# Optimization experiments

Measured on AMD Instinct MI355X. Metric: run time of the kernel, lower is better.

## Reference

```python
import jax, jax.numpy as jnp
import numpy as np

N = 100000  # num nodes
E = 1600000  # num edges
D_IN = 64
D_OUT = 64


def setup_inputs() -> dict:
    key = jax.random.key(0)
    k = jax.random.split(key, 8)
    x = jax.random.normal(k[0], (N, D_IN), dtype=jnp.float32)
    edge_index = jax.random.randint(k[1], (2, E), 0, N, dtype=jnp.int64)
    s1 = 1.0 / np.sqrt(D_IN)
    s2 = 1.0 / np.sqrt(D_OUT)
    W1 = jax.random.uniform(k[2], (D_IN, D_OUT), jnp.float32, -s1, s1)
    b1 = jax.random.uniform(k[3], (D_OUT,), jnp.float32, -s1, s1)
    W2 = jax.random.uniform(k[4], (D_OUT, D_OUT), jnp.float32, -s2, s2)
    b2 = jax.random.uniform(k[5], (D_OUT,), jnp.float32, -s2, s2)
    eps = jnp.asarray(0.0, dtype=jnp.float32)  # learnable (train_eps=True)
    return {"x": x, "edge_index": edge_index, "W1": W1, "b1": b1, "W2": W2, "b2": b2, "eps": eps}


def reference(x, edge_index, W1, b1, W2, b2, eps):
    src, dst = edge_index[0], edge_index[1]
    # sum-aggregate neighbor features: agg[i] = sum_{(j->i)} x[j]
    agg = jax.ops.segment_sum(x[src], dst, num_segments=N)  # [N, D_IN]
    h = (1.0 + eps) * x + agg
    h = jax.nn.relu(h @ W1 + b1)
    return h @ W2 + b2
```

## Files before the change

kernel.cpp:

```cpp
#include <hip/hip_runtime.h>

#define NN 100000
#define NE 1600000
#define D  64
#define NBK 512
#define NPB 196
#define CAP 4096
#define CHUNK 8192
#define NCH ((NE + CHUNK - 1) / CHUNK)


typedef unsigned short u16;
typedef __attribute__((ext_vector_type(8))) short bf16x8;
typedef __attribute__((ext_vector_type(4))) float f32x4;

__device__ __forceinline__ u16 f32_to_bf16_rn(float f) {
    unsigned u = __float_as_uint(f);
    return (u16)((u + 0x7FFF + ((u >> 16) & 1)) >> 16);
}
__device__ __forceinline__ float bf16_to_f32(u16 h) {
    return __uint_as_float(((unsigned)h) << 16);
}

__global__ __launch_bounds__(256) void cvt_kernel(const float* __restrict__ x,
                                                  u16* __restrict__ xb) {
    int i = (blockIdx.x * blockDim.x + threadIdx.x) * 4;
    if (i < NN * D) {
        float4 v = *(const float4*)(x + i);
        ushort4 o;
        o.x = f32_to_bf16_rn(v.x);
        o.y = f32_to_bf16_rn(v.y);
        o.z = f32_to_bf16_rn(v.z);
        o.w = f32_to_bf16_rn(v.w);
        *(ushort4*)(xb + i) = o;
    }
}

__global__ __launch_bounds__(256) void bin_kernel(const int* __restrict__ ei,
                                                  int* __restrict__ cursor,
                                                  int* __restrict__ bins) {
    __shared__ int lc[NBK];
    __shared__ int lbase[NBK];
    const int t = threadIdx.x;
    const int base = blockIdx.x * CHUNK;

    for (int i = t; i < NBK; i += 256) lc[i] = 0;
    __syncthreads();
    #pragma unroll 4
    for (int j = 0; j < CHUNK / 256; ++j) {
        int e = base + t + j * 256;
        if (e < NE) atomicAdd(&lc[(unsigned)ei[NE + e] / NPB], 1);
    }
    __syncthreads();
    for (int i = t; i < NBK; i += 256) {
        int c = lc[i];
        lbase[i] = c ? atomicAdd(&cursor[i], c) : 0;
        lc[i] = 0;
    }
    __syncthreads();
    #pragma unroll 4
    for (int j = 0; j < CHUNK / 256; ++j) {
        int e = base + t + j * 256;
        if (e < NE) {
            int src = ei[e];
            int dst = ei[NE + e];
            int b   = (unsigned)dst / NPB;
            int loc = dst - b * NPB;
            int o   = atomicAdd(&lc[b], 1);
            int pos = lbase[b] + o;
            if (pos < CAP)
                bins[b * CAP + pos] = (loc << 17) | src;
        }
    }
}

__global__ __launch_bounds__(1024) void agg_kernel(const float* __restrict__ x,
                                                   const u16* __restrict__ xb,
                                                   const float* __restrict__ eps,
                                                   const int* __restrict__ cursor,
                                                   const int* __restrict__ bins,
                                                   float* __restrict__ out) {
    __shared__ int sorted[CAP];
    __shared__ int tmp[256];
    __shared__ int off[256];
    __shared__ int cur[256];
    const int b    = blockIdx.x;
    const int t    = threadIdx.x;
    const int lane = t & 63;
    const int w    = t >> 6;
    const int base = b * CAP;
    const int n    = min(cursor[b], CAP);
    const float e1 = 1.0f + *eps;

    if (t < 256) tmp[t] = 0;
    __syncthreads();
    for (int i = t; i < n; i += 1024)
        atomicAdd(&tmp[bins[base + i] >> 17], 1);
    __syncthreads();
    int v = (t < 256) ? tmp[t] : 0;
    for (int o = 1; o < 256; o <<= 1) {
        int u = (t < 256 && t >= o) ? tmp[t - o] : 0;
        __syncthreads();
        if (t < 256) tmp[t] += u;
        __syncthreads();
    }
    if (t < 256) { off[t] = tmp[t] - v; cur[t] = tmp[t] - v; }
    __syncthreads();
    for (int i = t; i < n; i += 1024) {
        int pk  = bins[base + i];
        int pos = atomicAdd(&cur[pk >> 17], 1);
        sorted[pos] = pk & 0x1FFFF;
    }
    __syncthreads();

    #pragma unroll
    for (int j = 0; j < 13; ++j) {
        int r = w + 16 * j;
        if (r < NPB) {
            int node = b * NPB + r;
            if (node < NN) {
                float a = e1 * x[node * D + lane];
                int p  = off[r];
                int pe = off[r + 1];
                for (; p + 4 <= pe; p += 4) {
                    int i0 = sorted[p],     i1 = sorted[p + 1];
                    int i2 = sorted[p + 2], i3 = sorted[p + 3];
                    float v0 = bf16_to_f32(xb[i0 * D + lane]);
                    float v1 = bf16_to_f32(xb[i1 * D + lane]);
                    float v2 = bf16_to_f32(xb[i2 * D + lane]);
                    float v3 = bf16_to_f32(xb[i3 * D + lane]);
                    a += (v0 + v1) + (v2 + v3);
                }
                for (; p < pe; ++p) a += bf16_to_f32(xb[sorted[p] * D + lane]);
                out[node * D + lane] = a;
            }
        }
    }
}

__global__ __launch_bounds__(256, 2) void mlp_mfma_kernel(
        float* __restrict__ h,
        const float* __restrict__ W1, const float* __restrict__ b1,
        const float* __restrict__ W2, const float* __restrict__ b2) {
    __shared__ u16 lds[4][16 * 72];
    const int lane = threadIdx.x & 63;
    const int wv   = threadIdx.x >> 6;
    const int m    = lane & 15;
    const int q    = lane >> 4;
    u16* tile = &lds[wv][0];

    bf16x8 wb1[4][2], wb2[4][2];
    #pragma unroll
    for (int t = 0; t < 4; ++t)
        #pragma unroll
        for (int s = 0; s < 2; ++s) {
            bf16x8 f1, f2;
            #pragma unroll
            for (int j = 0; j < 8; ++j) {
                int k = s * 32 + q * 8 + j;
                int nn = t * 16 + m;
                f1[j] = (short)f32_to_bf16_rn(W1[k * D + nn]);
                f2[j] = (short)f32_to_bf16_rn(W2[k * D + nn]);
            }
            wb1[t][s] = f1;
            wb2[t][s] = f2;
        }
    float bias1[4], bias2[4];
    #pragma unroll
    for (int t = 0; t < 4; ++t) {
        bias1[t] = b1[t * 16 + m];
        bias2[t] = b2[t * 16 + m];
    }

    const int wave = blockIdx.x * 4 + wv;
    const int nw   = gridDim.x * 4;
    for (int ti = wave; ti < NN / 16; ti += nw) {
        const int rowbase = ti * 16;

        bf16x8 a1f[2];
        #pragma unroll
        for (int s = 0; s < 2; ++s) {
            const float* p = h + (rowbase + m) * D + s * 32 + q * 8;
            float4 v0 = *(const float4*)p;
            float4 v1 = *(const float4*)(p + 4);
            bf16x8 f;
            f[0] = (short)f32_to_bf16_rn(v0.x);
            f[1] = (short)f32_to_bf16_rn(v0.y);
            f[2] = (short)f32_to_bf16_rn(v0.z);
            f[3] = (short)f32_to_bf16_rn(v0.w);
            f[4] = (short)f32_to_bf16_rn(v1.x);
            f[5] = (short)f32_to_bf16_rn(v1.y);
            f[6] = (short)f32_to_bf16_rn(v1.z);
            f[7] = (short)f32_to_bf16_rn(v1.w);
            a1f[s] = f;
        }

        #pragma unroll
        for (int t = 0; t < 4; ++t) {
            f32x4 c = {0.f, 0.f, 0.f, 0.f};
            c = __builtin_amdgcn_mfma_f32_16x16x32_bf16(a1f[0], wb1[t][0], c, 0, 0, 0);
            c = __builtin_amdgcn_mfma_f32_16x16x32_bf16(a1f[1], wb1[t][1], c, 0, 0, 0);
            #pragma unroll
            for (int r = 0; r < 4; ++r) {
                float vv = fmaxf(c[r] + bias1[t], 0.0f);
                tile[(q * 4 + r) * 72 + t * 16 + m] = f32_to_bf16_rn(vv);
            }
        }

        bf16x8 a2f[2];
        #pragma unroll
        for (int s = 0; s < 2; ++s)
            a2f[s] = *(const bf16x8*)&tile[m * 72 + s * 32 + q * 8];

        #pragma unroll
        for (int t = 0; t < 4; ++t) {
            f32x4 c = {0.f, 0.f, 0.f, 0.f};
            c = __builtin_amdgcn_mfma_f32_16x16x32_bf16(a2f[0], wb2[t][0], c, 0, 0, 0);
            c = __builtin_amdgcn_mfma_f32_16x16x32_bf16(a2f[1], wb2[t][1], c, 0, 0, 0);
            #pragma unroll
            for (int r = 0; r < 4; ++r)
                h[(rowbase + q * 4 + r) * D + t * 16 + m] = c[r] + bias2[t];
        }
    }
}

extern "C" void kernel_launch(void* const* d_in, const int* in_sizes, int n_in,
                              void* d_out, int out_size, void* d_ws, size_t ws_size,
                              hipStream_t stream) {
    const float* x   = (const float*)d_in[0];
    const int*   ei  = (const int*)d_in[1];
    const float* W1  = (const float*)d_in[2];
    const float* b1  = (const float*)d_in[3];
    const float* W2  = (const float*)d_in[4];
    const float* b2  = (const float*)d_in[5];
    const float* eps = (const float*)d_in[6];
    float*       out = (float*)d_out;

    int* cursor = (int*)d_ws;
    int* bins   = cursor + NBK;
    u16* xb     = (u16*)(bins + NBK * CAP);

    hipMemsetAsync(cursor, 0, NBK * sizeof(int), stream);
    cvt_kernel<<<(NN * D / 4 + 255) / 256, 256, 0, stream>>>(x, xb);
    bin_kernel<<<NCH, 256, 0, stream>>>(ei, cursor, bins);
    agg_kernel<<<NBK, 1024, 0, stream>>>(x, xb, eps, cursor, bins, out);
    mlp_mfma_kernel<<<1024, 256, 0, stream>>>(out, W1, b1, W2, b2);
}
```

Baseline: 181.2 us.

## Gather four neighbor rows per wave with vectorized loads and shuffle reduction

The aggregation inner loop now splits each wave into four 16-lane groups, each loading a full 64-element bf16 neighbor row as ushort4 per lane. Four edges are processed concurrently, and the partial sums are combined with xor shuffles before one group writes float4 output. This replaces scalar 2-byte per-lane gathers, aiming for wider memory transactions and more loads in flight, at the cost of shuffles and masked tail work. The binning chunk size is also cut to 8192/4 per block with full unrolling, giving more blocks for the bin kernel.

```diff
diff --git a/kernel.cpp b/kernel.cpp
--- a/kernel.cpp
+++ b/kernel.cpp
@@ -6,7 +6,7 @@
 #define NBK 512
 #define NPB 196
 #define CAP 4096
-#define CHUNK 8192
+#define CHUNK 2048
 #define NCH ((NE + CHUNK - 1) / CHUNK)
 
 
@@ -46,7 +46,7 @@
 
     for (int i = t; i < NBK; i += 256) lc[i] = 0;
     __syncthreads();
-    #pragma unroll 4
+    #pragma unroll
     for (int j = 0; j < CHUNK / 256; ++j) {
         int e = base + t + j * 256;
         if (e < NE) atomicAdd(&lc[(unsigned)ei[NE + e] / NPB], 1);
@@ -58,7 +58,7 @@
         lc[i] = 0;
     }
     __syncthreads();
-    #pragma unroll 4
+    #pragma unroll
     for (int j = 0; j < CHUNK / 256; ++j) {
         int e = base + t + j * 256;
         if (e < NE) {
@@ -113,26 +113,42 @@
     }
     __syncthreads();
 
+    const int g = lane >> 4;
+    const int m = lane & 15;
     #pragma unroll
     for (int j = 0; j < 13; ++j) {
         int r = w + 16 * j;
         if (r < NPB) {
             int node = b * NPB + r;
             if (node < NN) {
-                float a = e1 * x[node * D + lane];
-                int p  = off[r];
-                int pe = off[r + 1];
-                for (; p + 4 <= pe; p += 4) {
-                    int i0 = sorted[p],     i1 = sorted[p + 1];
-                    int i2 = sorted[p + 2], i3 = sorted[p + 3];
-                    float v0 = bf16_to_f32(xb[i0 * D + lane]);
-                    float v1 = bf16_to_f32(xb[i1 * D + lane]);
-                    float v2 = bf16_to_f32(xb[i2 * D + lane]);
-                    float v3 = bf16_to_f32(xb[i3 * D + lane]);
-                    a += (v0 + v1) + (v2 + v3);
+                float4 acc = {0.f, 0.f, 0.f, 0.f};
+                const int pe = off[r + 1];
+                for (int p = off[r]; p < pe; p += 4) {
+                    int pi  = p + g;
+                    int src = sorted[pi < pe ? pi : p];
+                    ushort4 u = *(const ushort4*)(xb + src * D + 4 * m);
+                    float sel = (pi < pe) ? 1.0f : 0.0f;
+                    acc.x = fmaf(sel, bf16_to_f32(u.x), acc.x);
+                    acc.y = fmaf(sel, bf16_to_f32(u.y), acc.y);
+                    acc.z = fmaf(sel, bf16_to_f32(u.z), acc.z);
+                    acc.w = fmaf(sel, bf16_to_f32(u.w), acc.w);
                 }
-                for (; p < pe; ++p) a += bf16_to_f32(xb[sorted[p] * D + lane]);
-                out[node * D + lane] = a;
+                acc.x += __shfl_xor(acc.x, 16, 64);
+                acc.y += __shfl_xor(acc.y, 16, 64);
+                acc.z += __shfl_xor(acc.z, 16, 64);
+                acc.w += __shfl_xor(acc.w, 16, 64);
+                acc.x += __shfl_xor(acc.x, 32, 64);
+                acc.y += __shfl_xor(acc.y, 32, 64);
+                acc.z += __shfl_xor(acc.z, 32, 64);
+                acc.w += __shfl_xor(acc.w, 32, 64);
+                if (g == 0) {
+                    float4 s = *(const float4*)(x + node * D + 4 * m);
+                    acc.x = fmaf(e1, s.x, acc.x);
+                    acc.y = fmaf(e1, s.y, acc.y);
+                    acc.z = fmaf(e1, s.z, acc.z);
+                    acc.w = fmaf(e1, s.w, acc.w);
+                    *(float4*)(out + node * D + 4 * m) = acc;
+                }
             }
         }
     }
```

Result: no change. 184.2 us (+1.7%).
